# Optimization experiments

Measured on AMD Instinct MI355X. Metric: run time of the kernel, lower is better.

The kernel has to match this reference:

```python
import jax, jax.numpy as jnp
import numpy as np

HIDDEN = 1024
HEADS = 16
HEAD_DIM = HIDDEN // HEADS

def setup_inputs() -> dict:
    key = jax.random.key(0)
    k1, k2, k3 = jax.random.split(key, 3)
    scale = 1.0 / np.sqrt(HIDDEN)
    return {
        "x": jax.random.normal(k1, (2, 2048, HIDDEN), dtype=jnp.float32),
        "w_qkv": jax.random.normal(k2, (HIDDEN, 3 * HIDDEN), dtype=jnp.float32) * scale,
        "b_qkv": jnp.zeros((3 * HIDDEN,), dtype=jnp.float32),
        "w_out": jax.random.normal(k3, (HIDDEN, HIDDEN), dtype=jnp.float32) * scale,
        "b_out": jnp.zeros((HIDDEN,), dtype=jnp.float32),
    }

def reference(x, w_qkv, b_qkv, w_out, b_out):
    B, S, H = x.shape
    qkv = x @ w_qkv + b_qkv                              # (B,S,3H)
    qkv = qkv.reshape(B, S, 3, HEADS, HEAD_DIM)
    qkv = jnp.transpose(qkv, (2, 0, 3, 1, 4))            # (3,B,nh,S,hd)
    q, k, v = qkv[0], qkv[1], qkv[2]
    scores = jnp.einsum("bhqd,bhkd->bhqk", q, k) / np.sqrt(HEAD_DIM)
    causal = jnp.triu(jnp.ones((S, S), dtype=bool), k=1)  # True above diagonal
    scores = jnp.where(causal, -jnp.inf, scores)
    attn = jax.nn.softmax(scores, axis=-1)               # dropout: eval mode (identity)
    out = jnp.einsum("bhqk,bhkd->bhqd", attn, v)
    out = jnp.transpose(out, (0, 2, 1, 3)).reshape(B, S, H)
    return out @ w_out + b_out
```

## Files before the change

kernel.cpp:

```cpp
#include <hip/hip_runtime.h>
#include <hip/hip_bf16.h>

typedef short short8 __attribute__((ext_vector_type(8)));
typedef float f32x4 __attribute__((ext_vector_type(4)));

typedef const __attribute__((address_space(1))) unsigned int* gas_ptr;
typedef __attribute__((address_space(3))) unsigned int* las_ptr;
#define ASYNC16(g, l) __builtin_amdgcn_global_load_lds((gas_ptr)(g), (las_ptr)(l), 16, 0, 0)

__device__ __forceinline__ unsigned short f2bf(float f) {
    unsigned int u = __builtin_bit_cast(unsigned int, f);
    u += 0x7fff + ((u >> 16) & 1);
    return (unsigned short)(u >> 16);
}
__device__ __forceinline__ float bf2f(unsigned short s) {
    unsigned int u = (unsigned int)s << 16;
    return __builtin_bit_cast(float, u);
}
__device__ __forceinline__ unsigned int pkbf_trunc(float lo, float hi) {
    return __builtin_amdgcn_perm(__builtin_bit_cast(unsigned int, hi),
                                 __builtin_bit_cast(unsigned int, lo), 0x07060302u);
}

__device__ __forceinline__ void transpose_tile(
    const float* __restrict__ w, unsigned short* __restrict__ wt,
    int K, int N, int k0, int n0, unsigned short* tile)
{
    for (int i = threadIdx.x; i < 64 * 64; i += 256) {
        int r = i >> 6, c = i & 63;
        tile[r * 65 + c] = f2bf(w[(size_t)(k0 + r) * N + n0 + c]);
    }
    __syncthreads();
    for (int i = threadIdx.x; i < 64 * 64; i += 256) {
        int r = i >> 6, c = i & 63;
        wt[(size_t)(n0 + r) * K + k0 + c] = tile[c * 65 + r];
    }
}

__global__ __launch_bounds__(256) void prep(
    const float* __restrict__ x, const float* __restrict__ w_qkv,
    const float* __restrict__ w_out,
    unsigned short* __restrict__ x_b, unsigned short* __restrict__ wqkv_t,
    unsigned short* __restrict__ wout_t)
{
    __shared__ unsigned short tile[64 * 65];
    int bid = blockIdx.x;
    if (bid < 4096) {
        int i = (bid * 256 + threadIdx.x) * 4;
        float4 v = *(const float4*)(x + i);
        ushort4 o;
        o.x = f2bf(v.x); o.y = f2bf(v.y); o.z = f2bf(v.z); o.w = f2bf(v.w);
        *(ushort4*)(x_b + i) = o;
    } else if (bid < 4096 + 768) {
        int t = bid - 4096;
        transpose_tile(w_qkv, wqkv_t, 1024, 3072, (t / 48) * 64, (t % 48) * 64, tile);
    } else {
        int t = bid - 4864;
        transpose_tile(w_out, wout_t, 1024, 1024, (t >> 4) * 64, (t & 15) * 64, tile);
    }
}


template<bool OUT_BF16, bool QKV>
__global__ __launch_bounds__(256, 3) void gemm_bt(
    const unsigned short* __restrict__ A,
    const unsigned short* __restrict__ Bt,
    const float* __restrict__ bias,
    void* __restrict__ C,
    unsigned short* __restrict__ vTp,
    int M, int N, int K)
{
    __shared__ __align__(16) unsigned short As[128 * 32];
    __shared__ __align__(16) unsigned short Bs[128 * 32];
    const int tid = threadIdx.x;
    const int lane = tid & 63;
    const int wave = tid >> 6;
    const int wr = wave >> 1, wc = wave & 1;
    const int m0 = blockIdx.x * 128, n0 = blockIdx.y * 128;
    const int fr = lane & 15, fq = lane >> 4;

    f32x4 acc[4][4] = {};

    const int grow = lane >> 2;
    const int gcol = (lane & 3) * 8;
    const unsigned short* Ag = A  + (size_t)(m0 + wave * 32 + grow) * K + gcol;
    const unsigned short* Bg = Bt + (size_t)(n0 + wave * 32 + grow) * K + gcol;
    unsigned short* AsW0 = As + (wave * 32) * 32;
    unsigned short* AsW1 = As + (wave * 32 + 16) * 32;
    unsigned short* BsW0 = Bs + (wave * 32) * 32;
    unsigned short* BsW1 = Bs + (wave * 32 + 16) * 32;

    for (int k0 = 0; k0 < K; k0 += 32) {
        __syncthreads();
        ASYNC16(Ag + k0,          AsW0);
        ASYNC16(Ag + 16 * K + k0, AsW1);
        ASYNC16(Bg + k0,          BsW0);
        ASYNC16(Bg + 16 * K + k0, BsW1);
        __syncthreads();

        short8 af[4], bfr[4];
#pragma unroll
        for (int i = 0; i < 4; i++)
            af[i] = *(const short8*)(As + (wr * 64 + i * 16 + fr) * 32 + fq * 8);
#pragma unroll
        for (int j = 0; j < 4; j++)
            bfr[j] = *(const short8*)(Bs + (wc * 64 + j * 16 + fr) * 32 + fq * 8);
#pragma unroll
        for (int i = 0; i < 4; i++)
#pragma unroll
            for (int j = 0; j < 4; j++)
                acc[i][j] = __builtin_amdgcn_mfma_f32_16x16x32_bf16(af[i], bfr[j], acc[i][j], 0, 0, 0);
    }

#pragma unroll
    for (int i = 0; i < 4; i++)
#pragma unroll
        for (int j = 0; j < 4; j++) {
            int col = n0 + wc * 64 + j * 16 + fr;
            float bv = bias[col];
            if (QKV && col >= 2048) {
                int hh = (col - 2048) >> 6, d = col & 63;
#pragma unroll
                for (int r = 0; r < 4; r++) {
                    int row = m0 + wr * 64 + i * 16 + fq * 4 + r;
                    int bb = row >> 11, s = row & 2047;
                    vTp[((size_t)(bb * 16 + hh) * 64 + d) * 2048 + s] = f2bf(acc[i][j][r] + bv);
                }
            } else {
                const int cstride = QKV ? 2048 : N;
#pragma unroll
                for (int r = 0; r < 4; r++) {
                    int row = m0 + wr * 64 + i * 16 + fq * 4 + r;
                    float v = acc[i][j][r] + bv;
                    if (OUT_BF16)
                        ((unsigned short*)C)[(size_t)row * cstride + col] = f2bf(v);
                    else
                        ((float*)C)[(size_t)row * cstride + col] = v;
                }
            }
        }
}


template<int RG0>
__device__ __forceinline__ void attn_step(
    const unsigned short* __restrict__ Ks0, const unsigned short* __restrict__ Ks1,
    const unsigned short* __restrict__ Vs0, const unsigned short* __restrict__ Vs1,
    unsigned short* __restrict__ Psw,
    const short8 (&qf)[4][2], const short8 ones,
    f32x4 (&o_acc)[4][4], f32x4 (&l_acc)[4],
    int j0, int fr, int fq,
    const int (&qrow0)[4], bool diagA, bool diagB)
{
    short8 kf[4][2];
#pragma unroll
    for (int t = 0; t < 4; t++) {
        kf[t][0] = *(const short8*)(Ks0 + (t * 16 + fr) * 32 + fq * 8);
        kf[t][1] = *(const short8*)(Ks1 + (t * 16 + fr) * 32 + fq * 8);
    }

#pragma unroll
    for (int rg = RG0; rg < 4; rg++) {
        f32x4 s[4];
#pragma unroll
        for (int t = 0; t < 4; t++) {
            s[t] = (f32x4){0.f, 0.f, 0.f, 0.f};
            s[t] = __builtin_amdgcn_mfma_f32_16x16x32_bf16(qf[rg][0], kf[t][0], s[t], 0, 0, 0);
            s[t] = __builtin_amdgcn_mfma_f32_16x16x32_bf16(qf[rg][1], kf[t][1], s[t], 0, 0, 0);
        }
        const bool diag = (rg < 2) ? diagA : diagB;
        unsigned short* prow = Psw + rg * (16 * 64);
        if (diag) {
#pragma unroll
            for (int t = 0; t < 4; t++) {
                float p[4];
#pragma unroll
                for (int r = 0; r < 4; r++) {
                    float v = __expf(s[t][r] * 0.125f - 8.0f);
                    if ((j0 + t * 16 + fr) > (qrow0[rg] + fq * 4 + r)) v = 0.f;
                    p[r] = v;
                }
                unsigned int pk01 = pkbf_trunc(p[0], p[1]);
                unsigned int pk23 = pkbf_trunc(p[2], p[3]);
                int base = (fq * 4) * 64 + ((t * 16 + fr + 16 * fq) & 63);
                prow[base]       = (unsigned short)pk01;
                prow[base + 64]  = (unsigned short)(pk01 >> 16);
                prow[base + 128] = (unsigned short)pk23;
                prow[base + 192] = (unsigned short)(pk23 >> 16);
            }
        } else {
#pragma unroll
            for (int t = 0; t < 4; t++) {
                float p[4];
#pragma unroll
                for (int r = 0; r < 4; r++)
                    p[r] = __expf(s[t][r] * 0.125f - 8.0f);
                unsigned int pk01 = pkbf_trunc(p[0], p[1]);
                unsigned int pk23 = pkbf_trunc(p[2], p[3]);
                int base = (fq * 4) * 64 + ((t * 16 + fr + 16 * fq) & 63);
                prow[base]       = (unsigned short)pk01;
                prow[base + 64]  = (unsigned short)(pk01 >> 16);
                prow[base + 128] = (unsigned short)pk23;
                prow[base + 192] = (unsigned short)(pk23 >> 16);
            }
        }
    }

#pragma unroll
    for (int ks = 0; ks < 2; ks++) {
        const unsigned short* Vsb = ks ? Vs1 : Vs0;
        const int colp = (ks * 32 + fq * 8 + 16 * ((fr >> 2) & 3)) & 63;
        short8 pf[4];
#pragma unroll
        for (int rg = RG0; rg < 4; rg++)
            pf[rg] = *(const short8*)(Psw + rg * (16 * 64) + fr * 64 + colp);
#pragma unroll
        for (int t = 0; t < 4; t++) {
            short8 vf = *(const short8*)(Vsb + (t * 16 + fr) * 32 + fq * 8);
#pragma unroll
            for (int rg = RG0; rg < 4; rg++)
                o_acc[rg][t] = __builtin_amdgcn_mfma_f32_16x16x32_bf16(pf[rg], vf, o_acc[rg][t], 0, 0, 0);
        }
#pragma unroll
        for (int rg = RG0; rg < 4; rg++)
            l_acc[rg] = __builtin_amdgcn_mfma_f32_16x16x32_bf16(pf[rg], ones, l_acc[rg], 0, 0, 0);
    }
}

__global__ __launch_bounds__(128, 2) void flash_attn(
    const unsigned short* __restrict__ qkv,
    const unsigned short* __restrict__ vT,
    unsigned short* __restrict__ Opart,
    float* __restrict__ lpart)
{
    const int p = blockIdx.x;
    const int g = blockIdx.y;
    const int h = blockIdx.z & 15, b = blockIdx.z >> 4;
    const int tid = threadIdx.x, wave = tid >> 6, lane = tid & 63;
    const int fr = lane & 15, fq = lane >> 4;
    const size_t RS = 2048;

    const unsigned short* Qb = qkv + (size_t)b * 2048 * RS + h * 64;
    const unsigned short* Kb = Qb + 1024;
    const unsigned short* Vt = vT + (size_t)(b * 16 + h) * 64 * 2048;

    __shared__ __align__(16) unsigned short Ks[2][64 * 32];
    __shared__ __align__(16) unsigned short Vs[2][64 * 32];
    __shared__ __align__(16) unsigned short Ps[2][4 * 16 * 64];

    short8 qf[4][2];
    int qrow0[4];
#pragma unroll
    for (int rg = 0; rg < 4; rg++) {
        int qt = (rg < 2) ? p : (31 - p);
        qrow0[rg] = qt * 64 + wave * 32 + (rg & 1) * 16;
        const unsigned short* qrow = Qb + (size_t)(qrow0[rg] + fr) * RS;
        qf[rg][0] = *(const short8*)(qrow + fq * 8);
        qf[rg][1] = *(const short8*)(qrow + 32 + fq * 8);
    }
    short8 ones;
#pragma unroll
    for (int e = 0; e < 8; e++) ones[e] = (short)0x3F80;

    f32x4 o_acc[4][4] = {};
    f32x4 l_acc[4] = {};

    const int grow = lane >> 2;
    const int gcol = (lane & 3) * 8;
    const unsigned short* Kg = Kb + (size_t)(wave * 32 + grow) * RS + gcol;
    const unsigned short* Vg = Vt + (size_t)(wave * 32 + grow) * 2048 + gcol;
    unsigned short* KsW00 = Ks[0] + (wave * 32) * 32;
    unsigned short* KsW01 = Ks[0] + (wave * 32 + 16) * 32;
    unsigned short* KsW10 = Ks[1] + (wave * 32) * 32;
    unsigned short* KsW11 = Ks[1] + (wave * 32 + 16) * 32;
    unsigned short* VsW00 = Vs[0] + (wave * 32) * 32;
    unsigned short* VsW01 = Vs[0] + (wave * 32 + 16) * 32;
    unsigned short* VsW10 = Vs[1] + (wave * 32) * 32;
    unsigned short* VsW11 = Vs[1] + (wave * 32 + 16) * 32;

    const int mid = (p >= 8) ? 8 : (16 - p);
    const int lo = g ? mid : 0;
    const int hi = g ? (32 - p) : mid;

    for (int jt = lo; jt < hi; jt++) {
        const int j0 = jt * 64;
        __syncthreads();
        ASYNC16(Kg + (size_t)j0 * RS,               KsW00);
        ASYNC16(Kg + (size_t)(j0 + 16) * RS,        KsW01);
        ASYNC16(Kg + (size_t)j0 * RS + 32,          KsW10);
        ASYNC16(Kg + (size_t)(j0 + 16) * RS + 32,   KsW11);
        ASYNC16(Vg + j0,               VsW00);
        ASYNC16(Vg + 16 * 2048 + j0,   VsW01);
        ASYNC16(Vg + j0 + 32,          VsW10);
        ASYNC16(Vg + 16 * 2048 + j0 + 32, VsW11);
        __syncthreads();

        bool diagA = (jt == p), diagB = (jt == 31 - p);
        if (jt <= p)
            attn_step<0>(Ks[0], Ks[1], Vs[0], Vs[1], Ps[wave], qf, ones,
                         o_acc, l_acc, j0, fr, fq, qrow0, diagA, diagB);
        else
            attn_step<2>(Ks[0], Ks[1], Vs[0], Vs[1], Ps[wave], qf, ones,
                         o_acc, l_acc, j0, fr, fq, qrow0, diagA, diagB);
    }

    unsigned short* Og = Opart + (size_t)g * 4096 * 1024;
    float* lg = lpart + (size_t)g * 4096 * 16;
#pragma unroll
    for (int rg = 0; rg < 4; rg++) {
#pragma unroll
        for (int t = 0; t < 4; t++)
#pragma unroll
            for (int r = 0; r < 4; r++) {
                int row = qrow0[rg] + fq * 4 + r;
                Og[(size_t)(b * 2048 + row) * 1024 + h * 64 + t * 16 + fr] = f2bf(o_acc[rg][t][r]);
            }
        if (fr == 0) {
#pragma unroll
            for (int r = 0; r < 4; r++) {
                int row = qrow0[rg] + fq * 4 + r;
                lg[(size_t)(b * 2048 + row) * 16 + h] = l_acc[rg][r];
            }
        }
    }
}

__global__ __launch_bounds__(256) void reduce_attn(
    const unsigned short* __restrict__ Opart, const float* __restrict__ lpart,
    unsigned short* __restrict__ out)
{
    int i = (blockIdx.x * 256 + threadIdx.x) * 8;
    int row = i >> 10, h = (i & 1023) >> 6;
    float lsum = lpart[(size_t)row * 16 + h] + lpart[(size_t)4096 * 16 + row * 16 + h];
    float inv = 1.0f / lsum;
    ushort4 a0 = *(const ushort4*)(Opart + i);
    ushort4 a1 = *(const ushort4*)(Opart + i + 4);
    ushort4 b0 = *(const ushort4*)(Opart + (size_t)4096 * 1024 + i);
    ushort4 b1 = *(const ushort4*)(Opart + (size_t)4096 * 1024 + i + 4);
    ushort4 o0, o1;
    o0.x = f2bf((bf2f(a0.x) + bf2f(b0.x)) * inv);
    o0.y = f2bf((bf2f(a0.y) + bf2f(b0.y)) * inv);
    o0.z = f2bf((bf2f(a0.z) + bf2f(b0.z)) * inv);
    o0.w = f2bf((bf2f(a0.w) + bf2f(b0.w)) * inv);
    o1.x = f2bf((bf2f(a1.x) + bf2f(b1.x)) * inv);
    o1.y = f2bf((bf2f(a1.y) + bf2f(b1.y)) * inv);
    o1.z = f2bf((bf2f(a1.z) + bf2f(b1.z)) * inv);
    o1.w = f2bf((bf2f(a1.w) + bf2f(b1.w)) * inv);
    *(ushort4*)(out + i) = o0;
    *(ushort4*)(out + i + 4) = o1;
}

extern "C" void kernel_launch(void* const* d_in, const int* in_sizes, int n_in,
                              void* d_out, int out_size, void* d_ws, size_t ws_size,
                              hipStream_t stream) {
    const float* x      = (const float*)d_in[0];
    const float* w_qkv  = (const float*)d_in[1];
    const float* b_qkv  = (const float*)d_in[2];
    const float* w_out  = (const float*)d_in[3];
    const float* b_out  = (const float*)d_in[4];
    float* out = (float*)d_out;

    char* ws = (char*)d_ws;
    unsigned short* x_b    = (unsigned short*)(ws);
    unsigned short* wqkv_t = (unsigned short*)(ws + 8u  * 1024 * 1024);
    unsigned short* wout_t = (unsigned short*)(ws + 14u * 1024 * 1024);
    unsigned short* qkv    = (unsigned short*)(ws + 16u * 1024 * 1024);
    unsigned short* attn   = (unsigned short*)(ws + 32u * 1024 * 1024);
    unsigned short* vT     = (unsigned short*)(ws + 40u * 1024 * 1024);
    unsigned short* Opart  = (unsigned short*)(ws + 48u * 1024 * 1024);
    float*          lpart  = (float*)         (ws + 64u * 1024 * 1024);

    prep<<<5120, 256, 0, stream>>>(x, w_qkv, w_out, x_b, wqkv_t, wout_t);
    gemm_bt<true, true ><<<dim3(32, 24), 256, 0, stream>>>(x_b,  wqkv_t, b_qkv, qkv, vT, 4096, 3072, 1024);
    flash_attn<<<dim3(16, 2, 32), 128, 0, stream>>>(qkv, vT, Opart, lpart);
    reduce_attn<<<2048, 256, 0, stream>>>(Opart, lpart, attn);
    gemm_bt<false, false><<<dim3(32, 8),  256, 0, stream>>>(attn, wout_t, b_out, out, nullptr, 4096, 1024, 1024);
}
```

Baseline: 193.0 us.

## Split flash attention KV range into three balanced-cost chunks per query pair

The flash attention grid moves from two KV splits per paired query tile to three. Each split's KV range is chosen by walking a cost model that counts diagonal-region tiles double, so the three chunks carry similar work. The launch is flattened to 1536 blocks with batch/head in the low bits, and the reduce kernel now sums three partials. The workspace is re-laid out so Opart overlaps the dead x_b/wqkv_t buffers. This adds more partial output traffic and reduce work in exchange for better load balance and more blocks across the CUs.

```diff
diff --git a/kernel.cpp b/kernel.cpp
--- a/kernel.cpp
+++ b/kernel.cpp
@@ -233,9 +233,12 @@
     unsigned short* __restrict__ Opart,
     float* __restrict__ lpart)
 {
-    const int p = blockIdx.x;
-    const int g = blockIdx.y;
-    const int h = blockIdx.z & 15, b = blockIdx.z >> 4;
+    const int gid = blockIdx.x;
+    const int bh = gid & 31;
+    const int sl = gid >> 5;
+    const int p  = sl & 15;
+    const int g  = sl >> 4;
+    const int h = bh & 15, b = bh >> 4;
     const int tid = threadIdx.x, wave = tid >> 6, lane = tid & 63;
     const int fr = lane & 15, fq = lane >> 4;
     const size_t RS = 2048;
@@ -278,9 +281,18 @@
     unsigned short* VsW10 = Vs[1] + (wave * 32) * 32;
     unsigned short* VsW11 = Vs[1] + (wave * 32 + 16) * 32;
 
-    const int mid = (p >= 8) ? 8 : (16 - p);
-    const int lo = g ? mid : 0;
-    const int hi = g ? (32 - p) : mid;
+    const int njt = 32 - p;
+    int lo = (g == 0) ? 0 : njt;
+    int hi = njt;
+    {
+        int cum = 0;
+        bool flo = (g == 0), fhi = false;
+        for (int j = 0; j < njt; j++) {
+            if (!flo && cum >= 44 * g)        { lo = j; flo = true; }
+            if (!fhi && cum >= 44 * (g + 1))  { hi = j; fhi = true; }
+            cum += (j <= p) ? 8 : 4;
+        }
+    }
 
     for (int jt = lo; jt < hi; jt++) {
         const int j0 = jt * 64;
@@ -329,23 +341,26 @@
     const unsigned short* __restrict__ Opart, const float* __restrict__ lpart,
     unsigned short* __restrict__ out)
 {
+    const size_t OP = (size_t)4096 * 1024, LP = (size_t)4096 * 16;
     int i = (blockIdx.x * 256 + threadIdx.x) * 8;
     int row = i >> 10, h = (i & 1023) >> 6;
-    float lsum = lpart[(size_t)row * 16 + h] + lpart[(size_t)4096 * 16 + row * 16 + h];
+    float lsum = lpart[row * 16 + h] + lpart[LP + row * 16 + h] + lpart[2 * LP + row * 16 + h];
     float inv = 1.0f / lsum;
-    ushort4 a0 = *(const ushort4*)(Opart + i);
-    ushort4 a1 = *(const ushort4*)(Opart + i + 4);
-    ushort4 b0 = *(const ushort4*)(Opart + (size_t)4096 * 1024 + i);
-    ushort4 b1 = *(const ushort4*)(Opart + (size_t)4096 * 1024 + i + 4);
+    float acc[8];
+#pragma unroll
+    for (int e = 0; e < 8; e++) acc[e] = 0.f;
+#pragma unroll
+    for (int gpart = 0; gpart < 3; gpart++) {
+        ushort4 a0 = *(const ushort4*)(Opart + gpart * OP + i);
+        ushort4 a1 = *(const ushort4*)(Opart + gpart * OP + i + 4);
+        acc[0] += bf2f(a0.x); acc[1] += bf2f(a0.y); acc[2] += bf2f(a0.z); acc[3] += bf2f(a0.w);
+        acc[4] += bf2f(a1.x); acc[5] += bf2f(a1.y); acc[6] += bf2f(a1.z); acc[7] += bf2f(a1.w);
+    }
     ushort4 o0, o1;
-    o0.x = f2bf((bf2f(a0.x) + bf2f(b0.x)) * inv);
-    o0.y = f2bf((bf2f(a0.y) + bf2f(b0.y)) * inv);
-    o0.z = f2bf((bf2f(a0.z) + bf2f(b0.z)) * inv);
-    o0.w = f2bf((bf2f(a0.w) + bf2f(b0.w)) * inv);
-    o1.x = f2bf((bf2f(a1.x) + bf2f(b1.x)) * inv);
-    o1.y = f2bf((bf2f(a1.y) + bf2f(b1.y)) * inv);
-    o1.z = f2bf((bf2f(a1.z) + bf2f(b1.z)) * inv);
-    o1.w = f2bf((bf2f(a1.w) + bf2f(b1.w)) * inv);
+    o0.x = f2bf(acc[0] * inv); o0.y = f2bf(acc[1] * inv);
+    o0.z = f2bf(acc[2] * inv); o0.w = f2bf(acc[3] * inv);
+    o1.x = f2bf(acc[4] * inv); o1.y = f2bf(acc[5] * inv);
+    o1.z = f2bf(acc[6] * inv); o1.w = f2bf(acc[7] * inv);
     *(ushort4*)(out + i) = o0;
     *(ushort4*)(out + i + 4) = o1;
 }
@@ -361,18 +376,19 @@
     float* out = (float*)d_out;
 
     char* ws = (char*)d_ws;
-    unsigned short* x_b    = (unsigned short*)(ws);
-    unsigned short* wqkv_t = (unsigned short*)(ws + 8u  * 1024 * 1024);
-    unsigned short* wout_t = (unsigned short*)(ws + 14u * 1024 * 1024);
-    unsigned short* qkv    = (unsigned short*)(ws + 16u * 1024 * 1024);
-    unsigned short* attn   = (unsigned short*)(ws + 32u * 1024 * 1024);
-    unsigned short* vT     = (unsigned short*)(ws + 40u * 1024 * 1024);
-    unsigned short* Opart  = (unsigned short*)(ws + 48u * 1024 * 1024);
-    float*          lpart  = (float*)         (ws + 64u * 1024 * 1024);
+    const size_t MB = 1024 * 1024;
+    unsigned short* qkv    = (unsigned short*)(ws);
+    unsigned short* vT     = (unsigned short*)(ws + 16 * MB);
+    unsigned short* wout_t = (unsigned short*)(ws + 24 * MB);
+    unsigned short* attn   = (unsigned short*)(ws + 26 * MB);
+    float*          lpart  = (float*)         (ws + 34 * MB);
+    unsigned short* x_b    = (unsigned short*)(ws + 36 * MB);
+    unsigned short* wqkv_t = (unsigned short*)(ws + 44 * MB);
+    unsigned short* Opart  = (unsigned short*)(ws + 36 * MB);
 
     prep<<<5120, 256, 0, stream>>>(x, w_qkv, w_out, x_b, wqkv_t, wout_t);
     gemm_bt<true, true ><<<dim3(32, 24), 256, 0, stream>>>(x_b,  wqkv_t, b_qkv, qkv, vT, 4096, 3072, 1024);
-    flash_attn<<<dim3(16, 2, 32), 128, 0, stream>>>(qkv, vT, Opart, lpart);
+    flash_attn<<<1536, 128, 0, stream>>>(qkv, vT, Opart, lpart);
     reduce_attn<<<2048, 256, 0, stream>>>(Opart, lpart, attn);
     gemm_bt<false, false><<<dim3(32, 8),  256, 0, stream>>>(attn, wout_t, b_out, out, nullptr, 4096, 1024, 1024);
 }
```

New measurement: 196.9 us. +2.0%, slower.
